# Kernel tuning notes

Hardware: AMD Instinct MI355X
Metric: run time of the kernel (lower is better)

Reference implementation:

```python
import jax, jax.numpy as jnp
import numpy as np

N = 96        # num_nodes
D = 64        # emb_size / n_hid
BS = 16
T = 13
G = 1         # num_graph

# all N^2 ordered pairs, receiver-major: edge e=i*N+j has receiver i, sender j
_REC = jnp.repeat(jnp.arange(N), N)
_SEND = jnp.tile(jnp.arange(N), N)


def _lin(shape, key, scale=0.05):
    return (jax.random.normal(key, shape, dtype=jnp.float32) * scale)


def setup_inputs() -> dict:
    key = jax.random.key(0)
    ks = jax.random.split(key, 24)
    inp = {
        "skill_seq": jax.random.randint(ks[0], (BS, T), 0, N, dtype=jnp.int32),
        "adj": jax.random.uniform(ks[1], (G, BS, N, N), dtype=jnp.float32),
        "node_embeddings": jax.random.normal(ks[2], (G, N, D), dtype=jnp.float32),
        # edge MLP
        "W_msg1": _lin((2 * D, D), ks[3]), "b_msg1": jnp.zeros((D,), jnp.float32),
        "W_msg2": _lin((D, D), ks[4]),     "b_msg2": jnp.zeros((D,), jnp.float32),
        # GRU hidden projections (no bias)
        "W_hr": _lin((D, D), ks[5]), "W_hi": _lin((D, D), ks[6]), "W_hh": _lin((D, D), ks[7]),
        # GRU input projections (bias)
        "W_ir": _lin((D, D), ks[8]),  "b_ir": jnp.zeros((D,), jnp.float32),
        "W_ii": _lin((D, D), ks[9]),  "b_ii": jnp.zeros((D,), jnp.float32),
        "W_in": _lin((D, D), ks[10]), "b_in": jnp.zeros((D,), jnp.float32),
        # output MLP
        "W_o1": _lin((D, D), ks[11]), "b_o1": jnp.zeros((D,), jnp.float32),
        "W_o2": _lin((D, D), ks[12]), "b_o2": jnp.zeros((D,), jnp.float32),
        "W_o3": _lin((D, D), ks[13]), "b_o3": jnp.zeros((D,), jnp.float32),
    }
    return inp


def _forward(skill_seq, adj, node_embeddings,
             W_msg1, b_msg1, W_msg2, b_msg2,
             W_hr, W_hi, W_hh,
             W_ir, b_ir, W_ii, b_ii, W_in, b_in,
             W_o1, b_o1, W_o2, b_o2, W_o3, b_o3):
    bs, time_steps = skill_seq.shape
    hidden0 = jnp.zeros((G, bs, N, D), dtype=adj.dtype)
    emb = node_embeddings[0]  # [N, D] (num_graph=1)

    def step(hidden, skill_t):
        # gather senders/receivers over the node axis -> [G, bs, N^2, 2D]
        senders = hidden[:, :, _SEND, :]
        receivers = hidden[:, :, _REC, :]
        pre_msg = jnp.concatenate([senders, receivers], axis=-1)
        msg = jnp.tanh(pre_msg @ W_msg1 + b_msg1)        # [G, bs, N^2, D]
        msg = jnp.tanh(msg @ W_msg2 + b_msg2)
        msg = msg.reshape(G, bs, N, N, D)                # receiver i, sender j
        # mask by adjacency and scatter-sum over senders, then /N
        agg = jnp.einsum('gbij,gbijd->gbid', adj, msg) / N   # [G, bs, N, D]
        inputs = emb[skill_t][None, :, None, :]          # [1, bs, 1, D]
        r = jax.nn.sigmoid(inputs @ W_ir + b_ir + agg @ W_hr)
        i = jax.nn.sigmoid(inputs @ W_ii + b_ii + agg @ W_hi)
        n = jnp.tanh(inputs @ W_in + b_in + r * (agg @ W_hh))
        hidden = (1.0 - i) * n + i * hidden
        pred = jax.nn.relu(hidden @ W_o1 + b_o1)
        pred = jax.nn.relu(pred @ W_o2 + b_o2)
        pred = pred @ W_o3 + b_o3                        # [G, bs, N, D]
        return hidden, pred

    skills_t = skill_seq[:, :time_steps - 1].T           # [T-1, bs]
    _, preds = jax.lax.scan(step, hidden0, skills_t)     # [T-1, G, bs, N, D]
    # torch: stack(dim=1) -> [G, T-1, bs, N, D]; transpose(1,2) -> [G, bs, T-1, N, D]
    return jnp.transpose(preds, (1, 2, 0, 3, 4))


def reference(skill_seq, adj, node_embeddings,
              W_msg1, b_msg1, W_msg2, b_msg2,
              W_hr, W_hi, W_hh,
              W_ir, b_ir, W_ii, b_ii, W_in, b_in,
              W_o1, b_o1, W_o2, b_o2, W_o3, b_o3):
    return _forward(skill_seq, adj, node_embeddings,
                    W_msg1, b_msg1, W_msg2, b_msg2,
                    W_hr, W_hi, W_hh,
                    W_ir, b_ir, W_ii, b_ii, W_in, b_in,
                    W_o1, b_o1, W_o2, b_o2, W_o3, b_o3)
```

## Files before the change

kernel.cpp:

```cpp
#include <hip/hip_runtime.h>

typedef unsigned short ushort_t;
typedef __attribute__((ext_vector_type(8))) short short8;
typedef __attribute__((ext_vector_type(8))) __bf16 bf16x8;
typedef __attribute__((ext_vector_type(4))) float floatx4;

#define NN 96
#define DD 64
#define BSZ 16
#define TSTEP 12
#define JSPLIT 8
#define JPW 12
#define ITILES 6

#define OFF_HALL  0u
#define OFF_E     5111808u
#define OFF_S0    5185536u
#define OFF_S1    5578752u
#define OFF_R0    5971968u
#define OFF_R1    6365184u
#define OFF_PART  6758400u
#define OFF_WSWZ  9904128u
#define OFF_CNT   9977856u
#define HSLOT     98304

union fragU  { short8 s; bf16x8 b; };
union packU  { floatx4 f; unsigned long long u[2]; };

static __device__ __forceinline__ short f2bf(float f){
    union { float f; unsigned u; } v; v.f = f;
    unsigned u = v.u;
    u += 0x7fffu + ((u >> 16) & 1u);
    return (short)(u >> 16);
}
static __device__ __forceinline__ float fast_tanh(float x){
    float p = __expf(2.f * x);
    return (p - 1.f) * __builtin_amdgcn_rcpf(p + 1.f);
}
static __device__ __forceinline__ float fast_sigmoid(float x){
    float p = __expf(-x);
    return __builtin_amdgcn_rcpf(1.f + p);
}
static __device__ __forceinline__ void zero4(floatx4* a){
    floatx4 z = {0.f,0.f,0.f,0.f};
    a[0]=z; a[1]=z; a[2]=z; a[3]=z;
}
static __device__ __forceinline__ void buildA(const float* sM, int col, int quad, short8& a0, short8& a1){
    floatx4 f0 = *(const floatx4*)&sM[col*68 + quad*8];
    floatx4 f1 = *(const floatx4*)&sM[col*68 + quad*8 + 4];
    floatx4 f2 = *(const floatx4*)&sM[col*68 + 32 + quad*8];
    floatx4 f3 = *(const floatx4*)&sM[col*68 + 32 + quad*8 + 4];
    fragU u0, u1;
    #pragma unroll
    for (int jj = 0; jj < 4; jj++){
        u0.b[jj]   = (__bf16)f0[jj];
        u0.b[4+jj] = (__bf16)f1[jj];
        u1.b[jj]   = (__bf16)f2[jj];
        u1.b[4+jj] = (__bf16)f3[jj];
    }
    a0 = u0.s; a1 = u1.s;
}
static __device__ __forceinline__ void mm16(short8 a0, short8 a1, const short8* wzm, int l, floatx4* acc){
    #pragma unroll
    for (int nt = 0; nt < 4; nt++){
        short8 b0 = wzm[nt*64 + l];
        short8 b1 = wzm[(4 + nt)*64 + l];
        acc[nt] = __builtin_amdgcn_mfma_f32_16x16x32_bf16(a0, b0, acc[nt], 0, 0, 0);
        acc[nt] = __builtin_amdgcn_mfma_f32_16x16x32_bf16(a1, b1, acc[nt], 0, 0, 0);
    }
}
static __device__ __forceinline__ void mm16r(short8 a0, short8 a1, const short8* f, floatx4* acc){
    #pragma unroll
    for (int nt = 0; nt < 4; nt++){
        acc[nt] = __builtin_amdgcn_mfma_f32_16x16x32_bf16(a0, f[nt],     acc[nt], 0, 0, 0);
        acc[nt] = __builtin_amdgcn_mfma_f32_16x16x32_bf16(a1, f[4 + nt], acc[nt], 0, 0, 0);
    }
}

__global__ __launch_bounds__(256) void k_init(
    const float* __restrict__ emb, const float* __restrict__ Wmsg1,
    const float* __restrict__ Wmsg2,
    const float* __restrict__ Whr, const float* __restrict__ Whi, const float* __restrict__ Whh,
    const float* __restrict__ Wir, const float* __restrict__ bir,
    const float* __restrict__ Wii, const float* __restrict__ bii,
    const float* __restrict__ Win, const float* __restrict__ bin,
    const float* __restrict__ Wo1, const float* __restrict__ Wo2, const float* __restrict__ Wo3,
    float* __restrict__ hz, float* __restrict__ S0, float* __restrict__ R0,
    int* __restrict__ cnt,
    float* __restrict__ Ef, ushort_t* __restrict__ wswz)
{
    int wg = blockIdx.x, tid = threadIdx.x;
    if (wg < 288) {
        int flat = wg*256 + tid;
        floatx4 z = {0.f,0.f,0.f,0.f};
        if      (flat < 24576) ((floatx4*)hz)[flat] = z;
        else if (flat < 49152) ((floatx4*)S0)[flat - 24576] = z;
        else                   ((floatx4*)R0)[flat - 49152] = z;
        if (wg < 5) {
            int c = wg*256 + tid;
            if (c < TSTEP*BSZ*ITILES) cnt[c] = 0;
        }
    } else if (wg < 360) {
        int flat = (wg - 288)*256 + tid;
        int m = flat / 6144; int r = flat % 6144; int s = r >> 6; int d = r & 63;
        const float* W = (m==0)? Wir : (m==1)? Wii : Win;
        const float* B = (m==0)? bir : (m==1)? bii : bin;
        float acc = B[d];
        #pragma unroll 8
        for (int k = 0; k < 64; k++)
            acc += emb[s*64 + k] * W[k*64 + d];
        Ef[flat] = acc;
    } else {
        int flat = (wg - 360)*256 + tid;
        int m = flat >> 12; int q = flat & 4095;
        int jj = q & 7, lane = (q >> 3) & 63, nt = (q >> 9) & 3, kc = q >> 11;
        int k = kc*32 + ((lane >> 4) << 3) + jj;
        int n = nt*16 + (lane & 15);
        const float* src; int idx = k*64 + n;
        switch (m) {
          case 0: src = Wmsg2; break;
          case 1: src = Whr;  break;
          case 2: src = Whi;  break;
          case 3: src = Whh;  break;
          case 4: src = Wmsg1; break;
          case 5: src = Wmsg1; idx = (64 + k)*64 + n; break;
          case 6: src = Wo1; break;
          case 7: src = Wo2; break;
          default: src = Wo3; break;
        }
        wswz[flat] = (ushort_t)f2bf(src[idx]);
    }
}

__global__ __launch_bounds__(256) void k_step(
    const float* __restrict__ adj, const float* __restrict__ b1in, const float* __restrict__ b2in,
    const float* __restrict__ Sread, const float* __restrict__ Rread,
    const ushort_t* __restrict__ wswz, float* __restrict__ partial,
    const int* __restrict__ skills, const float* __restrict__ Ef,
    const float* __restrict__ hprev, float* __restrict__ hcur,
    float* __restrict__ Swrite, float* __restrict__ Rwrite,
    int* __restrict__ cnt, int t)
{
    __shared__ float lds[6400];
    __shared__ int sLast;
    float* sS   = lds;
    float* sRB  = lds + 768;
    float* sAdj = lds + 1856;
    float* sAgg = lds + 2048;

    int wg = blockIdx.x;
    int js = wg / 96; int rem = wg % 96; int b = rem / 6; int it = rem % 6;
    int tid = threadIdx.x; int w = tid >> 6; int l = tid & 63;
    int quad = l >> 4, col = l & 15;
    int j0 = js * JPW;

    for (int q = tid; q < JPW*16; q += 256) {
        int row = q >> 4, c4 = (q & 15) * 4;
        *(floatx4*)&sS[row*64 + c4] = *(const floatx4*)&Sread[(b*NN + j0 + row)*64 + c4];
    }
    for (int q = tid; q < 16*16; q += 256) {
        int row = q >> 4, c4 = (q & 15) * 4;
        floatx4 r4 = *(const floatx4*)&Rread[(b*NN + it*16 + row)*64 + c4];
        floatx4 b4 = *(const floatx4*)&b1in[c4];
        floatx4 o = r4 + b4;
        *(floatx4*)&sRB[row*68 + c4] = o;
    }
    for (int q = tid; q < 16*JPW; q += 256) {
        int i = q / JPW, j = q % JPW;
        sAdj[q] = adj[(b*NN + it*16 + i)*NN + j0 + j];
    }
    const short8* wz = (const short8*)wswz;
    short8 w2f[2][4];
    #pragma unroll
    for (int kc = 0; kc < 2; kc++)
      #pragma unroll
      for (int nt = 0; nt < 4; nt++)
        w2f[kc][nt] = wz[(kc*4 + nt)*64 + l];
    float b2v[4];
    #pragma unroll
    for (int nt = 0; nt < 4; nt++) b2v[nt] = b2in[nt*16 + col];
    __syncthreads();

    float rbv[16];
    #pragma unroll
    for (int c = 0; c < 4; c++)
        *(floatx4*)&rbv[c*4] = *(const floatx4*)&sRB[col*68 + (c>>1)*32 + quad*8 + (c&1)*4];

    float agg[4][4];
    #pragma unroll
    for (int nt=0;nt<4;nt++)
      #pragma unroll
      for (int r=0;r<4;r++) agg[nt][r] = 0.f;

    for (int c = 0; c < 3; c++) {
        int jl = w*3 + c;
        float sv[16];
        #pragma unroll
        for (int cc = 0; cc < 4; cc++)
            *(floatx4*)&sv[cc*4] = *(const floatx4*)&sS[jl*64 + (cc>>1)*32 + quad*8 + (cc&1)*4];
        fragU u0, u1;
        #pragma unroll
        for (int e = 0; e < 8; e++) {
            u0.b[e] = (__bf16)fast_tanh(sv[e]   + rbv[e]);
            u1.b[e] = (__bf16)fast_tanh(sv[8+e] + rbv[8+e]);
        }
        floatx4 acc[4];
        zero4(acc);
        #pragma unroll
        for (int nt = 0; nt < 4; nt++) {
            acc[nt] = __builtin_amdgcn_mfma_f32_16x16x32_bf16(u0.s, w2f[0][nt], acc[nt], 0,0,0);
            acc[nt] = __builtin_amdgcn_mfma_f32_16x16x32_bf16(u1.s, w2f[1][nt], acc[nt], 0,0,0);
        }
        float adjv[4];
        #pragma unroll
        for (int r = 0; r < 4; r++) adjv[r] = sAdj[(quad*4 + r)*JPW + jl];
        #pragma unroll
        for (int nt = 0; nt < 4; nt++)
          #pragma unroll
          for (int r = 0; r < 4; r++)
            agg[nt][r] += adjv[r] * fast_tanh(acc[nt][r] + b2v[nt]);
    }
    #pragma unroll
    for (int nt = 0; nt < 4; nt++)
      #pragma unroll
      for (int r = 0; r < 4; r++)
        sAgg[w*1088 + (quad*4 + r)*68 + nt*16 + col] = agg[nt][r];
    __syncthreads();
    {
        int i = tid >> 4, k4 = (tid & 15) * 4;
        floatx4 s0 = *(const floatx4*)&sAgg[0*1088 + i*68 + k4];
        floatx4 s1 = *(const floatx4*)&sAgg[1*1088 + i*68 + k4];
        floatx4 s2 = *(const floatx4*)&sAgg[2*1088 + i*68 + k4];
        floatx4 s3 = *(const floatx4*)&sAgg[3*1088 + i*68 + k4];
        floatx4 o = (s0 + s1) + (s2 + s3);
        o = o * (1.f/96.f);
        packU pk; pk.f = o;
        unsigned long long* dst =
            (unsigned long long*)&partial[((js*BSZ + b)*NN + it*16 + i)*64 + k4];
        __hip_atomic_store(dst,     pk.u[0], __ATOMIC_RELAXED, __HIP_MEMORY_SCOPE_AGENT);
        __hip_atomic_store(dst + 1, pk.u[1], __ATOMIC_RELAXED, __HIP_MEMORY_SCOPE_AGENT);
    }
    if (t == TSTEP - 1) return;

    __syncthreads();
    if (tid == 0) {
        int old = atomicAdd(&cnt[t*(BSZ*ITILES) + b*ITILES + it], 1);
        sLast = (old == JSPLIT - 1);
    }
    __syncthreads();
    if (!sLast) return;

    float* sM = lds;
    float* sG = lds + 1088;
    float* sH = lds + 4352;
    float* sE = lds + 5376;

    const short8* wzb = (const short8*)wswz;
    short8 fG[8], fSR[8];
    if (w < 3) {
        #pragma unroll
        for (int q = 0; q < 8; q++) fG[q] = wzb[(1 + w)*512 + q*64 + l];
    }
    if (w < 2) {
        #pragma unroll
        for (int q = 0; q < 8; q++) fSR[q] = wzb[(4 + w)*512 + q*64 + l];
    }

    {
        int i = tid >> 4, k4 = (tid & 15) * 4;
        floatx4 a = {0.f,0.f,0.f,0.f};
        #pragma unroll
        for (int p = 0; p < JSPLIT; p++) {
            const unsigned long long* src =
                (const unsigned long long*)&partial[((p*BSZ + b)*NN + it*16 + i)*64 + k4];
            packU pk;
            pk.u[0] = __hip_atomic_load(src,     __ATOMIC_RELAXED, __HIP_MEMORY_SCOPE_AGENT);
            pk.u[1] = __hip_atomic_load(src + 1, __ATOMIC_RELAXED, __HIP_MEMORY_SCOPE_AGENT);
            a += pk.f;
        }
        *(floatx4*)&sM[i*68 + k4] = a;
        *(floatx4*)&sH[i*64 + k4] = *(const floatx4*)&hprev[(b*NN + it*16 + i)*64 + k4];
    }
    if (tid < 192) {
        int s = skills[b*13 + t];
        sE[tid] = Ef[(tid >> 6)*6144 + s*64 + (tid & 63)];
    }
    __syncthreads();

    if (w < 3) {
        short8 a0, a1;
        buildA(sM, col, quad, a0, a1);
        floatx4 acc[4];
        zero4(acc);
        mm16r(a0, a1, fG, acc);
        #pragma unroll
        for (int nt = 0; nt < 4; nt++)
          #pragma unroll
          for (int r = 0; r < 4; r++)
            sG[w*1088 + (quad*4 + r)*68 + nt*16 + col] = acc[nt][r];
    }
    __syncthreads();

    {
        int i = tid >> 4, k4 = (tid & 15) * 4;
        float h[4];
        #pragma unroll
        for (int e = 0; e < 4; e++) {
            int d = k4 + e;
            float gr = fast_sigmoid(sE[d]       + sG[0*1088 + i*68 + d]);
            float gi = fast_sigmoid(sE[64 + d]  + sG[1*1088 + i*68 + d]);
            float nv = fast_tanh  (sE[128 + d] + gr * sG[2*1088 + i*68 + d]);
            h[e] = (1.f - gi)*nv + gi*sH[i*64 + d];
        }
        #pragma unroll
        for (int e = 0; e < 4; e++) sM[i*68 + k4 + e] = h[e];
        floatx4 hv = { h[0], h[1], h[2], h[3] };
        *(floatx4*)&hcur[(b*NN + it*16 + i)*64 + k4] = hv;
    }
    __syncthreads();

    if (w < 2) {
        short8 a0, a1;
        buildA(sM, col, quad, a0, a1);
        floatx4 acc[4];
        zero4(acc);
        mm16r(a0, a1, fSR, acc);
        float* dst = (w == 0) ? Swrite : Rwrite;
        #pragma unroll
        for (int nt = 0; nt < 4; nt++)
          #pragma unroll
          for (int r = 0; r < 4; r++)
            dst[(b*NN + it*16 + quad*4 + r)*64 + nt*16 + col] = acc[nt][r];
    }
}

__global__ __launch_bounds__(256) void k_out(
    const int* __restrict__ skills, const float* __restrict__ partial,
    const float* __restrict__ Ef, const float* __restrict__ hall,
    const ushort_t* __restrict__ wswz,
    const float* __restrict__ bo1, const float* __restrict__ bo2, const float* __restrict__ bo3,
    float* __restrict__ out)
{
    __shared__ float sT[4][16*68];
    int tid = threadIdx.x; int w = tid >> 6; int l = tid & 63;
    int quad = l >> 4, col = l & 15;
    int g = blockIdx.x*4 + w;
    int ts = g / 96; int rem = g % 96; int b = rem / 6, it = rem % 6;
    float* sm = sT[w];

    if (ts < 11) {
        const float* hsrc = hall + (size_t)(ts + 1)*HSLOT + (b*NN + it*16)*64;
        int i = l >> 2, c0 = (l & 3)*16;
        #pragma unroll
        for (int cc = 0; cc < 4; cc++)
            *(floatx4*)&sm[i*68 + c0 + cc*4] = *(const floatx4*)&hsrc[i*64 + c0 + cc*4];
    } else {
        int i = l >> 2, c0 = (l & 3)*16;
        floatx4 a[4]; zero4(a);
        for (int p = 0; p < JSPLIT; p++) {
            const float* base = &partial[((p*BSZ + b)*NN + it*16 + i)*64 + c0];
            #pragma unroll
            for (int cc = 0; cc < 4; cc++) a[cc] += *(const floatx4*)&base[cc*4];
        }
        #pragma unroll
        for (int cc = 0; cc < 4; cc++) *(floatx4*)&sm[i*68 + c0 + cc*4] = a[cc];

        short8 a0, a1; buildA(sm, col, quad, a0, a1);
        floatx4 Ar[4], Ai[4], Ah[4];
        zero4(Ar); zero4(Ai); zero4(Ah);
        mm16(a0, a1, (const short8*)wswz + 1*512, l, Ar);
        mm16(a0, a1, (const short8*)wswz + 2*512, l, Ai);
        mm16(a0, a1, (const short8*)wswz + 3*512, l, Ah);
        int s = skills[b*13 + 11];
        const float* hp = hall + 11*(size_t)HSLOT;
        #pragma unroll
        for (int nt = 0; nt < 4; nt++) {
            int d = nt*16 + col;
            float er = Ef[0*6144 + s*64 + d];
            float ei = Ef[1*6144 + s*64 + d];
            float en = Ef[2*6144 + s*64 + d];
            #pragma unroll
            for (int r = 0; r < 4; r++) {
                int row = it*16 + quad*4 + r;
                float gr = fast_sigmoid(er + Ar[nt][r]);
                float gi = fast_sigmoid(ei + Ai[nt][r]);
                float nv = fast_tanh  (en + gr*Ah[nt][r]);
                sm[(quad*4 + r)*68 + d] = (1.f - gi)*nv + gi*hp[(b*NN + row)*64 + d];
            }
        }
    }

    float bv1[4], bv2[4], bv3[4];
    #pragma unroll
    for (int nt = 0; nt < 4; nt++) {
        bv1[nt] = bo1[nt*16 + col];
        bv2[nt] = bo2[nt*16 + col];
        bv3[nt] = bo3[nt*16 + col];
    }
    short8 a0, a1;
    floatx4 acc[4];

    buildA(sm, col, quad, a0, a1);
    zero4(acc);
    mm16(a0, a1, (const short8*)wswz + 6*512, l, acc);
    #pragma unroll
    for (int nt = 0; nt < 4; nt++)
      #pragma unroll
      for (int r = 0; r < 4; r++)
        sm[(quad*4 + r)*68 + nt*16 + col] = fmaxf(0.f, acc[nt][r] + bv1[nt]);

    buildA(sm, col, quad, a0, a1);
    zero4(acc);
    mm16(a0, a1, (const short8*)wswz + 7*512, l, acc);
    #pragma unroll
    for (int nt = 0; nt < 4; nt++)
      #pragma unroll
      for (int r = 0; r < 4; r++)
        sm[(quad*4 + r)*68 + nt*16 + col] = fmaxf(0.f, acc[nt][r] + bv2[nt]);

    buildA(sm, col, quad, a0, a1);
    zero4(acc);
    mm16(a0, a1, (const short8*)wswz + 8*512, l, acc);
    #pragma unroll
    for (int nt = 0; nt < 4; nt++)
      #pragma unroll
      for (int r = 0; r < 4; r++)
        out[((b*TSTEP + ts)*NN + it*16 + quad*4 + r)*64 + nt*16 + col] = acc[nt][r] + bv3[nt];
}

extern "C" void kernel_launch(void* const* d_in, const int* in_sizes, int n_in,
                              void* d_out, int out_size, void* d_ws, size_t ws_size,
                              hipStream_t stream) {
    const int*   skills = (const int*)d_in[0];
    const float* adj    = (const float*)d_in[1];
    const float* emb    = (const float*)d_in[2];
    const float* Wmsg1  = (const float*)d_in[3];
    const float* b1     = (const float*)d_in[4];
    const float* Wmsg2  = (const float*)d_in[5];
    const float* b2     = (const float*)d_in[6];
    const float* Whr    = (const float*)d_in[7];
    const float* Whi    = (const float*)d_in[8];
    const float* Whh    = (const float*)d_in[9];
    const float* Wir    = (const float*)d_in[10];
    const float* bir    = (const float*)d_in[11];
    const float* Wii    = (const float*)d_in[12];
    const float* bii    = (const float*)d_in[13];
    const float* Win    = (const float*)d_in[14];
    const float* bin    = (const float*)d_in[15];
    const float* Wo1    = (const float*)d_in[16];
    const float* bo1    = (const float*)d_in[17];
    const float* Wo2    = (const float*)d_in[18];
    const float* bo2    = (const float*)d_in[19];
    const float* Wo3    = (const float*)d_in[20];
    const float* bo3    = (const float*)d_in[21];

    char* ws = (char*)d_ws;
    float*    hall    = (float*)(ws + OFF_HALL);
    float*    Ef      = (float*)(ws + OFF_E);
    float*    S0      = (float*)(ws + OFF_S0);
    float*    S1      = (float*)(ws + OFF_S1);
    float*    R0      = (float*)(ws + OFF_R0);
    float*    R1      = (float*)(ws + OFF_R1);
    float*    partial = (float*)(ws + OFF_PART);
    ushort_t* wswz    = (ushort_t*)(ws + OFF_WSWZ);
    int*      cnt     = (int*)(ws + OFF_CNT);
    float*    out     = (float*)d_out;

    k_init<<<dim3(504), dim3(256), 0, stream>>>(emb, Wmsg1, Wmsg2, Whr, Whi, Whh,
        Wir, bir, Wii, bii, Win, bin, Wo1, Wo2, Wo3, hall, S0, R0, cnt, Ef, wswz);

    for (int t = 0; t < TSTEP; t++) {
        const float* Sr = (t & 1) ? S1 : S0;
        const float* Rr = (t & 1) ? R1 : R0;
        float*       Sw = (t & 1) ? S0 : S1;
        float*       Rw = (t & 1) ? R0 : R1;
        k_step<<<dim3(JSPLIT*BSZ*ITILES), dim3(256), 0, stream>>>(
            adj, b1, b2, Sr, Rr, wswz, partial, skills, Ef,
            hall + (size_t)t*HSLOT, hall + (size_t)(t+1)*HSLOT,
            Sw, Rw, cnt, t);
    }
    k_out<<<dim3(288), dim3(256), 0, stream>>>(skills, partial, Ef, hall, wswz,
        bo1, bo2, bo3, out);
}
```

Before: 255.5 us.

## Fuse per-timestep launches into one persistent kernel with tile-level flag synchronization

Replaces the twelve per-timestep k_step launches with a single persistent k_all kernel that loops over timesteps. Blocks wait on per-tile ready flags, published by the block that finishes the GRU update, instead of on kernel boundaries. S/R projections and hidden states are now kept per timestep rather than ping-ponged, and the initial zero state is synthesized in LDS. This removes launch gaps and full-grid barriers and lets independent tiles run ahead. The cost is spin-waiting, relaxed-atomic global traffic, and a reliance on all 768 blocks being co-resident (launch_bounds 256,3) to avoid deadlock.

```diff
diff --git a/kernel.cpp b/kernel.cpp
--- a/kernel.cpp
+++ b/kernel.cpp
@@ -12,16 +12,16 @@
 #define JSPLIT 8
 #define JPW 12
 #define ITILES 6
+#define NTILE (BSZ*ITILES)
 
 #define OFF_HALL  0u
 #define OFF_E     5111808u
-#define OFF_S0    5185536u
-#define OFF_S1    5578752u
-#define OFF_R0    5971968u
-#define OFF_R1    6365184u
-#define OFF_PART  6758400u
-#define OFF_WSWZ  9904128u
-#define OFF_CNT   9977856u
+#define OFF_SG    5185536u
+#define OFF_RG    9904128u
+#define OFF_PART  14622720u
+#define OFF_WSWZ  17768448u
+#define OFF_CNT   17842176u
+#define OFF_FLAG  17846784u
 #define HSLOT     98304
 
 union fragU  { short8 s; bf16x8 b; };
@@ -44,6 +44,19 @@
 static __device__ __forceinline__ void zero4(floatx4* a){
     floatx4 z = {0.f,0.f,0.f,0.f};
     a[0]=z; a[1]=z; a[2]=z; a[3]=z;
+}
+static __device__ __forceinline__ floatx4 aload4(const float* p){
+    const unsigned long long* s = (const unsigned long long*)p;
+    packU pk;
+    pk.u[0] = __hip_atomic_load(s,     __ATOMIC_RELAXED, __HIP_MEMORY_SCOPE_AGENT);
+    pk.u[1] = __hip_atomic_load(s + 1, __ATOMIC_RELAXED, __HIP_MEMORY_SCOPE_AGENT);
+    return pk.f;
+}
+static __device__ __forceinline__ void astore4(float* p, floatx4 v){
+    unsigned long long* d = (unsigned long long*)p;
+    packU pk; pk.f = v;
+    __hip_atomic_store(d,     pk.u[0], __ATOMIC_RELAXED, __HIP_MEMORY_SCOPE_AGENT);
+    __hip_atomic_store(d + 1, pk.u[1], __ATOMIC_RELAXED, __HIP_MEMORY_SCOPE_AGENT);
 }
 static __device__ __forceinline__ void buildA(const float* sM, int col, int quad, short8& a0, short8& a1){
     floatx4 f0 = *(const floatx4*)&sM[col*68 + quad*8];
@@ -85,23 +98,19 @@
     const float* __restrict__ Wii, const float* __restrict__ bii,
     const float* __restrict__ Win, const float* __restrict__ bin,
     const float* __restrict__ Wo1, const float* __restrict__ Wo2, const float* __restrict__ Wo3,
-    float* __restrict__ hz, float* __restrict__ S0, float* __restrict__ R0,
-    int* __restrict__ cnt,
+    float* __restrict__ hz, int* __restrict__ cntflag,
     float* __restrict__ Ef, ushort_t* __restrict__ wswz)
 {
     int wg = blockIdx.x, tid = threadIdx.x;
-    if (wg < 288) {
-        int flat = wg*256 + tid;
+    if (wg < 96) {
         floatx4 z = {0.f,0.f,0.f,0.f};
-        if      (flat < 24576) ((floatx4*)hz)[flat] = z;
-        else if (flat < 49152) ((floatx4*)S0)[flat - 24576] = z;
-        else                   ((floatx4*)R0)[flat - 49152] = z;
-        if (wg < 5) {
+        ((floatx4*)hz)[wg*256 + tid] = z;
+        if (wg < 9) {
             int c = wg*256 + tid;
-            if (c < TSTEP*BSZ*ITILES) cnt[c] = 0;
-        }
-    } else if (wg < 360) {
-        int flat = (wg - 288)*256 + tid;
+            if (c < 2304) cntflag[c] = 0;
+        }
+    } else if (wg < 168) {
+        int flat = (wg - 96)*256 + tid;
         int m = flat / 6144; int r = flat % 6144; int s = r >> 6; int d = r & 63;
         const float* W = (m==0)? Wir : (m==1)? Wii : Win;
         const float* B = (m==0)? bir : (m==1)? bii : bin;
@@ -111,7 +120,7 @@
             acc += emb[s*64 + k] * W[k*64 + d];
         Ef[flat] = acc;
     } else {
-        int flat = (wg - 360)*256 + tid;
+        int flat = (wg - 168)*256 + tid;
         int m = flat >> 12; int q = flat & 4095;
         int jj = q & 7, lane = (q >> 3) & 63, nt = (q >> 9) & 3, kc = q >> 11;
         int k = kc*32 + ((lane >> 4) << 3) + jj;
@@ -132,39 +141,31 @@
     }
 }
 
-__global__ __launch_bounds__(256) void k_step(
+__global__ __launch_bounds__(256, 3) void k_all(
     const float* __restrict__ adj, const float* __restrict__ b1in, const float* __restrict__ b2in,
-    const float* __restrict__ Sread, const float* __restrict__ Rread,
-    const ushort_t* __restrict__ wswz, float* __restrict__ partial,
     const int* __restrict__ skills, const float* __restrict__ Ef,
-    const float* __restrict__ hprev, float* __restrict__ hcur,
-    float* __restrict__ Swrite, float* __restrict__ Rwrite,
-    int* __restrict__ cnt, int t)
+    const ushort_t* __restrict__ wswz,
+    float* __restrict__ partial, float* __restrict__ Sbuf, float* __restrict__ Rbuf,
+    float* __restrict__ hall, int* __restrict__ cnt, int* __restrict__ flagv)
 {
-    __shared__ float lds[6400];
+    __shared__ float lds[7616];
     __shared__ int sLast;
     float* sS   = lds;
     float* sRB  = lds + 768;
     float* sAdj = lds + 1856;
     float* sAgg = lds + 2048;
+    float* sM = lds + 2048;
+    float* sG = lds + 3136;
+    float* sH = lds + 6400;
+    float* sE = lds + 7424;
 
     int wg = blockIdx.x;
     int js = wg / 96; int rem = wg % 96; int b = rem / 6; int it = rem % 6;
     int tid = threadIdx.x; int w = tid >> 6; int l = tid & 63;
     int quad = l >> 4, col = l & 15;
     int j0 = js * JPW;
-
-    for (int q = tid; q < JPW*16; q += 256) {
-        int row = q >> 4, c4 = (q & 15) * 4;
-        *(floatx4*)&sS[row*64 + c4] = *(const floatx4*)&Sread[(b*NN + j0 + row)*64 + c4];
-    }
-    for (int q = tid; q < 16*16; q += 256) {
-        int row = q >> 4, c4 = (q & 15) * 4;
-        floatx4 r4 = *(const floatx4*)&Rread[(b*NN + it*16 + row)*64 + c4];
-        floatx4 b4 = *(const floatx4*)&b1in[c4];
-        floatx4 o = r4 + b4;
-        *(floatx4*)&sRB[row*68 + c4] = o;
-    }
+    int jt0 = j0 >> 4, jt1 = (j0 + JPW - 1) >> 4;
+
     for (int q = tid; q < 16*JPW; q += 256) {
         int i = q / JPW, j = q % JPW;
         sAdj[q] = adj[(b*NN + it*16 + i)*NN + j0 + j];
@@ -179,158 +180,176 @@
     float b2v[4];
     #pragma unroll
     for (int nt = 0; nt < 4; nt++) b2v[nt] = b2in[nt*16 + col];
-    __syncthreads();
-
-    float rbv[16];
-    #pragma unroll
-    for (int c = 0; c < 4; c++)
-        *(floatx4*)&rbv[c*4] = *(const floatx4*)&sRB[col*68 + (c>>1)*32 + quad*8 + (c&1)*4];
-
-    float agg[4][4];
-    #pragma unroll
-    for (int nt=0;nt<4;nt++)
-      #pragma unroll
-      for (int r=0;r<4;r++) agg[nt][r] = 0.f;
-
-    for (int c = 0; c < 3; c++) {
-        int jl = w*3 + c;
-        float sv[16];
-        #pragma unroll
-        for (int cc = 0; cc < 4; cc++)
-            *(floatx4*)&sv[cc*4] = *(const floatx4*)&sS[jl*64 + (cc>>1)*32 + quad*8 + (cc&1)*4];
-        fragU u0, u1;
-        #pragma unroll
-        for (int e = 0; e < 8; e++) {
-            u0.b[e] = (__bf16)fast_tanh(sv[e]   + rbv[e]);
-            u1.b[e] = (__bf16)fast_tanh(sv[8+e] + rbv[8+e]);
-        }
-        floatx4 acc[4];
-        zero4(acc);
-        #pragma unroll
-        for (int nt = 0; nt < 4; nt++) {
-            acc[nt] = __builtin_amdgcn_mfma_f32_16x16x32_bf16(u0.s, w2f[0][nt], acc[nt], 0,0,0);
-            acc[nt] = __builtin_amdgcn_mfma_f32_16x16x32_bf16(u1.s, w2f[1][nt], acc[nt], 0,0,0);
-        }
-        float adjv[4];
-        #pragma unroll
-        for (int r = 0; r < 4; r++) adjv[r] = sAdj[(quad*4 + r)*JPW + jl];
+
+    for (int t = 0; t < TSTEP; t++) {
+        if (t == 0) {
+            for (int q = tid; q < JPW*64; q += 256) sS[q] = 0.f;
+            for (int q = tid; q < 16*64; q += 256) sRB[(q >> 6)*68 + (q & 63)] = b1in[q & 63];
+        } else {
+            if (tid < 3) {
+                int tile = (tid == 0) ? it : (tid == 1) ? jt0 : jt1;
+                const int* fp = &flagv[t*NTILE + b*ITILES + tile];
+                while (__hip_atomic_load(fp, __ATOMIC_RELAXED, __HIP_MEMORY_SCOPE_AGENT) == 0)
+                    __builtin_amdgcn_s_sleep(2);
+            }
+            __syncthreads();
+            const float* St = Sbuf + (size_t)t*HSLOT;
+            const float* Rt = Rbuf + (size_t)t*HSLOT;
+            for (int q = tid; q < JPW*16; q += 256) {
+                int row = q >> 4, c4 = (q & 15)*4;
+                *(floatx4*)&sS[row*64 + c4] = aload4(&St[(b*NN + j0 + row)*64 + c4]);
+            }
+            for (int q = tid; q < 16*16; q += 256) {
+                int row = q >> 4, c4 = (q & 15)*4;
+                floatx4 r4 = aload4(&Rt[(b*NN + it*16 + row)*64 + c4]);
+                floatx4 b4 = *(const floatx4*)&b1in[c4];
+                *(floatx4*)&sRB[row*68 + c4] = r4 + b4;
+            }
+        }
+        __syncthreads();
+
+        float rbv[16];
+        #pragma unroll
+        for (int c = 0; c < 4; c++)
+            *(floatx4*)&rbv[c*4] = *(const floatx4*)&sRB[col*68 + (c>>1)*32 + quad*8 + (c&1)*4];
+
+        float agg[4][4];
+        #pragma unroll
+        for (int nt=0;nt<4;nt++)
+          #pragma unroll
+          for (int r=0;r<4;r++) agg[nt][r] = 0.f;
+
+        for (int c = 0; c < 3; c++) {
+            int jl = w*3 + c;
+            float sv[16];
+            #pragma unroll
+            for (int cc = 0; cc < 4; cc++)
+                *(floatx4*)&sv[cc*4] = *(const floatx4*)&sS[jl*64 + (cc>>1)*32 + quad*8 + (cc&1)*4];
+            fragU u0, u1;
+            #pragma unroll
+            for (int e = 0; e < 8; e++) {
+                u0.b[e] = (__bf16)fast_tanh(sv[e]   + rbv[e]);
+                u1.b[e] = (__bf16)fast_tanh(sv[8+e] + rbv[8+e]);
+            }
+            floatx4 acc[4];
+            zero4(acc);
+            #pragma unroll
+            for (int nt = 0; nt < 4; nt++) {
+                acc[nt] = __builtin_amdgcn_mfma_f32_16x16x32_bf16(u0.s, w2f[0][nt], acc[nt], 0,0,0);
+                acc[nt] = __builtin_amdgcn_mfma_f32_16x16x32_bf16(u1.s, w2f[1][nt], acc[nt], 0,0,0);
+            }
+            float adjv[4];
+            #pragma unroll
+            for (int r = 0; r < 4; r++) adjv[r] = sAdj[(quad*4 + r)*JPW + jl];
+            #pragma unroll
+            for (int nt = 0; nt < 4; nt++)
+              #pragma unroll
+              for (int r = 0; r < 4; r++)
+                agg[nt][r] += adjv[r] * fast_tanh(acc[nt][r] + b2v[nt]);
+        }
         #pragma unroll
         for (int nt = 0; nt < 4; nt++)
           #pragma unroll
           for (int r = 0; r < 4; r++)
-            agg[nt][r] += adjv[r] * fast_tanh(acc[nt][r] + b2v[nt]);
-    }
-    #pragma unroll
-    for (int nt = 0; nt < 4; nt++)
-      #pragma unroll
-      for (int r = 0; r < 4; r++)
-        sAgg[w*1088 + (quad*4 + r)*68 + nt*16 + col] = agg[nt][r];
-    __syncthreads();
-    {
-        int i = tid >> 4, k4 = (tid & 15) * 4;
-        floatx4 s0 = *(const floatx4*)&sAgg[0*1088 + i*68 + k4];
-        floatx4 s1 = *(const floatx4*)&sAgg[1*1088 + i*68 + k4];
-        floatx4 s2 = *(const floatx4*)&sAgg[2*1088 + i*68 + k4];
-        floatx4 s3 = *(const floatx4*)&sAgg[3*1088 + i*68 + k4];
-        floatx4 o = (s0 + s1) + (s2 + s3);
-        o = o * (1.f/96.f);
-        packU pk; pk.f = o;
-        unsigned long long* dst =
-            (unsigned long long*)&partial[((js*BSZ + b)*NN + it*16 + i)*64 + k4];
-        __hip_atomic_store(dst,     pk.u[0], __ATOMIC_RELAXED, __HIP_MEMORY_SCOPE_AGENT);
-        __hip_atomic_store(dst + 1, pk.u[1], __ATOMIC_RELAXED, __HIP_MEMORY_SCOPE_AGENT);
-    }
-    if (t == TSTEP - 1) return;
-
-    __syncthreads();
-    if (tid == 0) {
-        int old = atomicAdd(&cnt[t*(BSZ*ITILES) + b*ITILES + it], 1);
-        sLast = (old == JSPLIT - 1);
-    }
-    __syncthreads();
-    if (!sLast) return;
-
-    float* sM = lds;
-    float* sG = lds + 1088;
-    float* sH = lds + 4352;
-    float* sE = lds + 5376;
-
-    const short8* wzb = (const short8*)wswz;
-    short8 fG[8], fSR[8];
-    if (w < 3) {
-        #pragma unroll
-        for (int q = 0; q < 8; q++) fG[q] = wzb[(1 + w)*512 + q*64 + l];
-    }
-    if (w < 2) {
-        #pragma unroll
-        for (int q = 0; q < 8; q++) fSR[q] = wzb[(4 + w)*512 + q*64 + l];
-    }
-
-    {
-        int i = tid >> 4, k4 = (tid & 15) * 4;
-        floatx4 a = {0.f,0.f,0.f,0.f};
-        #pragma unroll
-        for (int p = 0; p < JSPLIT; p++) {
-            const unsigned long long* src =
-                (const unsigned long long*)&partial[((p*BSZ + b)*NN + it*16 + i)*64 + k4];
-            packU pk;
-            pk.u[0] = __hip_atomic_load(src,     __ATOMIC_RELAXED, __HIP_MEMORY_SCOPE_AGENT);
-            pk.u[1] = __hip_atomic_load(src + 1, __ATOMIC_RELAXED, __HIP_MEMORY_SCOPE_AGENT);
-            a += pk.f;
-        }
-        *(floatx4*)&sM[i*68 + k4] = a;
-        *(floatx4*)&sH[i*64 + k4] = *(const floatx4*)&hprev[(b*NN + it*16 + i)*64 + k4];
-    }
-    if (tid < 192) {
-        int s = skills[b*13 + t];
-        sE[tid] = Ef[(tid >> 6)*6144 + s*64 + (tid & 63)];
-    }
-    __syncthreads();
-
-    if (w < 3) {
-        short8 a0, a1;
-        buildA(sM, col, quad, a0, a1);
-        floatx4 acc[4];
-        zero4(acc);
-        mm16r(a0, a1, fG, acc);
-        #pragma unroll
-        for (int nt = 0; nt < 4; nt++)
-          #pragma unroll
-          for (int r = 0; r < 4; r++)
-            sG[w*1088 + (quad*4 + r)*68 + nt*16 + col] = acc[nt][r];
-    }
-    __syncthreads();
-
-    {
-        int i = tid >> 4, k4 = (tid & 15) * 4;
-        float h[4];
-        #pragma unroll
-        for (int e = 0; e < 4; e++) {
-            int d = k4 + e;
-            float gr = fast_sigmoid(sE[d]       + sG[0*1088 + i*68 + d]);
-            float gi = fast_sigmoid(sE[64 + d]  + sG[1*1088 + i*68 + d]);
-            float nv = fast_tanh  (sE[128 + d] + gr * sG[2*1088 + i*68 + d]);
-            h[e] = (1.f - gi)*nv + gi*sH[i*64 + d];
-        }
-        #pragma unroll
-        for (int e = 0; e < 4; e++) sM[i*68 + k4 + e] = h[e];
-        floatx4 hv = { h[0], h[1], h[2], h[3] };
-        *(floatx4*)&hcur[(b*NN + it*16 + i)*64 + k4] = hv;
-    }
-    __syncthreads();
-
-    if (w < 2) {
-        short8 a0, a1;
-        buildA(sM, col, quad, a0, a1);
-        floatx4 acc[4];
-        zero4(acc);
-        mm16r(a0, a1, fSR, acc);
-        float* dst = (w == 0) ? Swrite : Rwrite;
-        #pragma unroll
-        for (int nt = 0; nt < 4; nt++)
-          #pragma unroll
-          for (int r = 0; r < 4; r++)
-            dst[(b*NN + it*16 + quad*4 + r)*64 + nt*16 + col] = acc[nt][r];
+            sAgg[w*1088 + (quad*4 + r)*68 + nt*16 + col] = agg[nt][r];
+        __syncthreads();
+        {
+            int i = tid >> 4, k4 = (tid & 15)*4;
+            floatx4 s0 = *(const floatx4*)&sAgg[0*1088 + i*68 + k4];
+            floatx4 s1 = *(const floatx4*)&sAgg[1*1088 + i*68 + k4];
+            floatx4 s2 = *(const floatx4*)&sAgg[2*1088 + i*68 + k4];
+            floatx4 s3 = *(const floatx4*)&sAgg[3*1088 + i*68 + k4];
+            floatx4 o = (s0 + s1) + (s2 + s3);
+            o = o * (1.f/96.f);
+            astore4(&partial[((js*BSZ + b)*NN + it*16 + i)*64 + k4], o);
+        }
+        if (t == TSTEP - 1) break;
+
+        __syncthreads();
+        if (tid == 0) {
+            int old = atomicAdd(&cnt[t*NTILE + b*ITILES + it], 1);
+            sLast = (old == JSPLIT - 1);
+        }
+        __syncthreads();
+
+        if (sLast) {
+            const short8* wzb = (const short8*)wswz;
+            short8 fG[8], fSR[8];
+            if (w < 3) {
+                #pragma unroll
+                for (int q = 0; q < 8; q++) fG[q] = wzb[(1 + w)*512 + q*64 + l];
+            }
+            if (w < 2) {
+                #pragma unroll
+                for (int q = 0; q < 8; q++) fSR[q] = wzb[(4 + w)*512 + q*64 + l];
+            }
+            {
+                int i = tid >> 4, k4 = (tid & 15)*4;
+                floatx4 a = {0.f,0.f,0.f,0.f};
+                #pragma unroll
+                for (int p = 0; p < JSPLIT; p++)
+                    a += aload4(&partial[((p*BSZ + b)*NN + it*16 + i)*64 + k4]);
+                *(floatx4*)&sM[i*68 + k4] = a;
+                *(floatx4*)&sH[i*64 + k4] =
+                    aload4(&hall[(size_t)t*HSLOT + (b*NN + it*16 + i)*64 + k4]);
+            }
+            if (tid < 192) {
+                int s = skills[b*13 + t];
+                sE[tid] = Ef[(tid >> 6)*6144 + s*64 + (tid & 63)];
+            }
+            __syncthreads();
+
+            if (w < 3) {
+                short8 a0, a1;
+                buildA(sM, col, quad, a0, a1);
+                floatx4 acc[4];
+                zero4(acc);
+                mm16r(a0, a1, fG, acc);
+                #pragma unroll
+                for (int nt = 0; nt < 4; nt++)
+                  #pragma unroll
+                  for (int r = 0; r < 4; r++)
+                    sG[w*1088 + (quad*4 + r)*68 + nt*16 + col] = acc[nt][r];
+            }
+            __syncthreads();
+
+            {
+                int i = tid >> 4, k4 = (tid & 15)*4;
+                float h[4];
+                #pragma unroll
+                for (int e = 0; e < 4; e++) {
+                    int d = k4 + e;
+                    float gr = fast_sigmoid(sE[d]       + sG[0*1088 + i*68 + d]);
+                    float gi = fast_sigmoid(sE[64 + d]  + sG[1*1088 + i*68 + d]);
+                    float nv = fast_tanh  (sE[128 + d] + gr * sG[2*1088 + i*68 + d]);
+                    h[e] = (1.f - gi)*nv + gi*sH[i*64 + d];
+                }
+                #pragma unroll
+                for (int e = 0; e < 4; e++) sM[i*68 + k4 + e] = h[e];
+                floatx4 hv = { h[0], h[1], h[2], h[3] };
+                astore4(&hall[(size_t)(t+1)*HSLOT + (b*NN + it*16 + i)*64 + k4], hv);
+            }
+            __syncthreads();
+
+            if (w < 2) {
+                short8 a0, a1;
+                buildA(sM, col, quad, a0, a1);
+                floatx4 acc[4];
+                zero4(acc);
+                mm16r(a0, a1, fSR, acc);
+                float* dst = ((w == 0) ? Sbuf : Rbuf) + (size_t)(t+1)*HSLOT;
+                #pragma unroll
+                for (int nt = 0; nt < 4; nt++)
+                  #pragma unroll
+                  for (int r = 0; r < 4; r++)
+                    __hip_atomic_store(&dst[(b*NN + it*16 + quad*4 + r)*64 + nt*16 + col],
+                                       acc[nt][r], __ATOMIC_RELAXED, __HIP_MEMORY_SCOPE_AGENT);
+            }
+            __syncthreads();
+            if (tid == 0)
+                __hip_atomic_store(&flagv[(t+1)*NTILE + b*ITILES + it], 1,
+                                   __ATOMIC_RELAXED, __HIP_MEMORY_SCOPE_AGENT);
+        }
     }
 }
 
@@ -457,28 +476,20 @@
     char* ws = (char*)d_ws;
     float*    hall    = (float*)(ws + OFF_HALL);
     float*    Ef      = (float*)(ws + OFF_E);
-    float*    S0      = (float*)(ws + OFF_S0);
-    float*    S1      = (float*)(ws + OFF_S1);
-    float*    R0      = (float*)(ws + OFF_R0);
-    float*    R1      = (float*)(ws + OFF_R1);
+    float*    Sbuf    = (float*)(ws + OFF_SG);
+    float*    Rbuf    = (float*)(ws + OFF_RG);
     float*    partial = (float*)(ws + OFF_PART);
     ushort_t* wswz    = (ushort_t*)(ws + OFF_WSWZ);
     int*      cnt     = (int*)(ws + OFF_CNT);
+    int*      flagv   = (int*)(ws + OFF_FLAG);
     float*    out     = (float*)d_out;
 
-    k_init<<<dim3(504), dim3(256), 0, stream>>>(emb, Wmsg1, Wmsg2, Whr, Whi, Whh,
-        Wir, bir, Wii, bii, Win, bin, Wo1, Wo2, Wo3, hall, S0, R0, cnt, Ef, wswz);
-
-    for (int t = 0; t < TSTEP; t++) {
-        const float* Sr = (t & 1) ? S1 : S0;
-        const float* Rr = (t & 1) ? R1 : R0;
-        float*       Sw = (t & 1) ? S0 : S1;
-        float*       Rw = (t & 1) ? R0 : R1;
-        k_step<<<dim3(JSPLIT*BSZ*ITILES), dim3(256), 0, stream>>>(
-            adj, b1, b2, Sr, Rr, wswz, partial, skills, Ef,
-            hall + (size_t)t*HSLOT, hall + (size_t)(t+1)*HSLOT,
-            Sw, Rw, cnt, t);
-    }
+    k_init<<<dim3(312), dim3(256), 0, stream>>>(emb, Wmsg1, Wmsg2, Whr, Whi, Whh,
+        Wir, bir, Wii, bii, Win, bin, Wo1, Wo2, Wo3, hall, cnt, Ef, wswz);
+
+    k_all<<<dim3(JSPLIT*BSZ*ITILES), dim3(256), 0, stream>>>(
+        adj, b1, b2, skills, Ef, wswz, partial, Sbuf, Rbuf, hall, cnt, flagv);
+
     k_out<<<dim3(288), dim3(256), 0, stream>>>(skills, partial, Ef, hall, wswz,
         bo1, bo2, bo3, out);
 }
```

After: 421.4 us. 65.0% more time.

## Specialize first recurrence step using zero initial hidden state

Applied to the files above, without the earlier changes.

Adds a dedicated k_step0 kernel that exploits the zero initial hidden state. Every edge message at step 0 is then the same vector, tanh(W2·tanh(b1)+b2), so aggregation reduces to adjacency row sums times that vector. This replaces a full 768-block edge-MLP pass with a 96-block kernel, and drops the zero-fill of hidden, S0 and R0 from k_init. It also fully unrolls the per-wave chunk loop in k_step and moves the atomic partial loads and stores into helpers. The risk is that any later read of the no-longer-zeroed hall slot 0 would see stale data.

```diff
diff --git a/kernel.cpp b/kernel.cpp
--- a/kernel.cpp
+++ b/kernel.cpp
@@ -45,6 +45,19 @@
     floatx4 z = {0.f,0.f,0.f,0.f};
     a[0]=z; a[1]=z; a[2]=z; a[3]=z;
 }
+static __device__ __forceinline__ floatx4 aload4(const float* p){
+    const unsigned long long* s = (const unsigned long long*)p;
+    packU pk;
+    pk.u[0] = __hip_atomic_load(s,     __ATOMIC_RELAXED, __HIP_MEMORY_SCOPE_AGENT);
+    pk.u[1] = __hip_atomic_load(s + 1, __ATOMIC_RELAXED, __HIP_MEMORY_SCOPE_AGENT);
+    return pk.f;
+}
+static __device__ __forceinline__ void astore4(float* p, floatx4 v){
+    unsigned long long* d = (unsigned long long*)p;
+    packU pk; pk.f = v;
+    __hip_atomic_store(d,     pk.u[0], __ATOMIC_RELAXED, __HIP_MEMORY_SCOPE_AGENT);
+    __hip_atomic_store(d + 1, pk.u[1], __ATOMIC_RELAXED, __HIP_MEMORY_SCOPE_AGENT);
+}
 static __device__ __forceinline__ void buildA(const float* sM, int col, int quad, short8& a0, short8& a1){
     floatx4 f0 = *(const floatx4*)&sM[col*68 + quad*8];
     floatx4 f1 = *(const floatx4*)&sM[col*68 + quad*8 + 4];
@@ -85,23 +98,11 @@
     const float* __restrict__ Wii, const float* __restrict__ bii,
     const float* __restrict__ Win, const float* __restrict__ bin,
     const float* __restrict__ Wo1, const float* __restrict__ Wo2, const float* __restrict__ Wo3,
-    float* __restrict__ hz, float* __restrict__ S0, float* __restrict__ R0,
-    int* __restrict__ cnt,
-    float* __restrict__ Ef, ushort_t* __restrict__ wswz)
+    int* __restrict__ cnt, float* __restrict__ Ef, ushort_t* __restrict__ wswz)
 {
     int wg = blockIdx.x, tid = threadIdx.x;
-    if (wg < 288) {
+    if (wg < 72) {
         int flat = wg*256 + tid;
-        floatx4 z = {0.f,0.f,0.f,0.f};
-        if      (flat < 24576) ((floatx4*)hz)[flat] = z;
-        else if (flat < 49152) ((floatx4*)S0)[flat - 24576] = z;
-        else                   ((floatx4*)R0)[flat - 49152] = z;
-        if (wg < 5) {
-            int c = wg*256 + tid;
-            if (c < TSTEP*BSZ*ITILES) cnt[c] = 0;
-        }
-    } else if (wg < 360) {
-        int flat = (wg - 288)*256 + tid;
         int m = flat / 6144; int r = flat % 6144; int s = r >> 6; int d = r & 63;
         const float* W = (m==0)? Wir : (m==1)? Wii : Win;
         const float* B = (m==0)? bir : (m==1)? bii : bin;
@@ -110,8 +111,12 @@
         for (int k = 0; k < 64; k++)
             acc += emb[s*64 + k] * W[k*64 + d];
         Ef[flat] = acc;
+        if (wg < 5) {
+            int c = wg*256 + tid;
+            if (c < TSTEP*BSZ*ITILES) cnt[c] = 0;
+        }
     } else {
-        int flat = (wg - 360)*256 + tid;
+        int flat = (wg - 72)*256 + tid;
         int m = flat >> 12; int q = flat & 4095;
         int jj = q & 7, lane = (q >> 3) & 63, nt = (q >> 9) & 3, kc = q >> 11;
         int k = kc*32 + ((lane >> 4) << 3) + jj;
@@ -132,6 +137,111 @@
     }
 }
 
+__global__ __launch_bounds__(256) void k_step0(
+    const float* __restrict__ adj, const float* __restrict__ b1in, const float* __restrict__ b2in,
+    const int* __restrict__ skills, const float* __restrict__ Ef,
+    const ushort_t* __restrict__ wswz,
+    float* __restrict__ hall, float* __restrict__ S1, float* __restrict__ R1)
+{
+    __shared__ float sM[16*68];
+    __shared__ float sG[3][16*68];
+    __shared__ float sE[3*64];
+    __shared__ float sRS[16*17];
+    int wg = blockIdx.x; int b = wg / 6, it = wg % 6;
+    int tid = threadIdx.x; int w = tid >> 6; int l = tid & 63;
+    int quad = l >> 4, col = l & 15;
+
+    {
+        int i = tid >> 4, seg = tid & 15;
+        const float* arow = &adj[(b*NN + it*16 + i)*NN + seg*6];
+        float s = 0.f;
+        #pragma unroll
+        for (int j = 0; j < 6; j++) s += arow[j];
+        sRS[i*17 + seg] = s;
+    }
+    if (tid < 192) {
+        int s = skills[b*13 + 0];
+        sE[tid] = Ef[(tid >> 6)*6144 + s*64 + (tid & 63)];
+    }
+    __syncthreads();
+    if (tid < 16) {
+        float s = 0.f;
+        #pragma unroll
+        for (int q = 0; q < 16; q++) s += sRS[tid*17 + q];
+        sRS[tid*17 + 16] = s * (1.f/96.f);
+    }
+    __syncthreads();
+
+    if (w == 0) {
+        float b2v[4];
+        #pragma unroll
+        for (int nt = 0; nt < 4; nt++) b2v[nt] = b2in[nt*16 + col];
+        fragU u0, u1;
+        #pragma unroll
+        for (int e = 0; e < 8; e++) {
+            u0.b[e] = (__bf16)fast_tanh(b1in[quad*8 + e]);
+            u1.b[e] = (__bf16)fast_tanh(b1in[32 + quad*8 + e]);
+        }
+        floatx4 acc[4];
+        zero4(acc);
+        mm16(u0.s, u1.s, (const short8*)wswz + 0*512, l, acc);
+        #pragma unroll
+        for (int nt = 0; nt < 4; nt++)
+          #pragma unroll
+          for (int r = 0; r < 4; r++) {
+            float m = fast_tanh(acc[nt][r] + b2v[nt]);
+            sM[(quad*4 + r)*68 + nt*16 + col] = sRS[(quad*4 + r)*17 + 16] * m;
+          }
+    }
+    __syncthreads();
+
+    if (w < 3) {
+        short8 a0, a1;
+        buildA(sM, col, quad, a0, a1);
+        floatx4 acc[4];
+        zero4(acc);
+        mm16(a0, a1, (const short8*)wswz + (1 + w)*512, l, acc);
+        #pragma unroll
+        for (int nt = 0; nt < 4; nt++)
+          #pragma unroll
+          for (int r = 0; r < 4; r++)
+            sG[w][(quad*4 + r)*68 + nt*16 + col] = acc[nt][r];
+    }
+    __syncthreads();
+
+    {
+        int i = tid >> 4, k4 = (tid & 15)*4;
+        float h[4];
+        #pragma unroll
+        for (int e = 0; e < 4; e++) {
+            int d = k4 + e;
+            float gi = fast_sigmoid(sE[64 + d] + sG[1][i*68 + d]);
+            float gr = fast_sigmoid(sE[d]      + sG[0][i*68 + d]);
+            float nv = fast_tanh  (sE[128 + d] + gr * sG[2][i*68 + d]);
+            h[e] = (1.f - gi)*nv;
+        }
+        #pragma unroll
+        for (int e = 0; e < 4; e++) sM[i*68 + k4 + e] = h[e];
+        floatx4 hv = { h[0], h[1], h[2], h[3] };
+        *(floatx4*)&hall[(size_t)1*HSLOT + (b*NN + it*16 + i)*64 + k4] = hv;
+    }
+    __syncthreads();
+
+    if (w < 2) {
+        short8 a0, a1;
+        buildA(sM, col, quad, a0, a1);
+        floatx4 acc[4];
+        zero4(acc);
+        mm16(a0, a1, (const short8*)wswz + (4 + w)*512, l, acc);
+        float* dst = (w == 0) ? S1 : R1;
+        #pragma unroll
+        for (int nt = 0; nt < 4; nt++)
+          #pragma unroll
+          for (int r = 0; r < 4; r++)
+            dst[(b*NN + it*16 + quad*4 + r)*64 + nt*16 + col] = acc[nt][r];
+    }
+}
+
 __global__ __launch_bounds__(256) void k_step(
     const float* __restrict__ adj, const float* __restrict__ b1in, const float* __restrict__ b2in,
     const float* __restrict__ Sread, const float* __restrict__ Rread,
@@ -192,6 +302,7 @@
       #pragma unroll
       for (int r=0;r<4;r++) agg[nt][r] = 0.f;
 
+    #pragma unroll
     for (int c = 0; c < 3; c++) {
         int jl = w*3 + c;
         float sv[16];
@@ -234,11 +345,7 @@
         floatx4 s3 = *(const floatx4*)&sAgg[3*1088 + i*68 + k4];
         floatx4 o = (s0 + s1) + (s2 + s3);
         o = o * (1.f/96.f);
-        packU pk; pk.f = o;
-        unsigned long long* dst =
-            (unsigned long long*)&partial[((js*BSZ + b)*NN + it*16 + i)*64 + k4];
-        __hip_atomic_store(dst,     pk.u[0], __ATOMIC_RELAXED, __HIP_MEMORY_SCOPE_AGENT);
-        __hip_atomic_store(dst + 1, pk.u[1], __ATOMIC_RELAXED, __HIP_MEMORY_SCOPE_AGENT);
+        astore4(&partial[((js*BSZ + b)*NN + it*16 + i)*64 + k4], o);
     }
     if (t == TSTEP - 1) return;
 
@@ -270,14 +377,8 @@
         int i = tid >> 4, k4 = (tid & 15) * 4;
         floatx4 a = {0.f,0.f,0.f,0.f};
         #pragma unroll
-        for (int p = 0; p < JSPLIT; p++) {
-            const unsigned long long* src =
-                (const unsigned long long*)&partial[((p*BSZ + b)*NN + it*16 + i)*64 + k4];
-            packU pk;
-            pk.u[0] = __hip_atomic_load(src,     __ATOMIC_RELAXED, __HIP_MEMORY_SCOPE_AGENT);
-            pk.u[1] = __hip_atomic_load(src + 1, __ATOMIC_RELAXED, __HIP_MEMORY_SCOPE_AGENT);
-            a += pk.f;
-        }
+        for (int p = 0; p < JSPLIT; p++)
+            a += aload4(&partial[((p*BSZ + b)*NN + it*16 + i)*64 + k4]);
         *(floatx4*)&sM[i*68 + k4] = a;
         *(floatx4*)&sH[i*64 + k4] = *(const floatx4*)&hprev[(b*NN + it*16 + i)*64 + k4];
     }
@@ -466,10 +567,13 @@
     int*      cnt     = (int*)(ws + OFF_CNT);
     float*    out     = (float*)d_out;
 
-    k_init<<<dim3(504), dim3(256), 0, stream>>>(emb, Wmsg1, Wmsg2, Whr, Whi, Whh,
-        Wir, bir, Wii, bii, Win, bin, Wo1, Wo2, Wo3, hall, S0, R0, cnt, Ef, wswz);
-
-    for (int t = 0; t < TSTEP; t++) {
+    k_init<<<dim3(216), dim3(256), 0, stream>>>(emb, Wmsg1, Wmsg2, Whr, Whi, Whh,
+        Wir, bir, Wii, bii, Win, bin, Wo1, Wo2, Wo3, cnt, Ef, wswz);
+
+    k_step0<<<dim3(BSZ*ITILES), dim3(256), 0, stream>>>(
+        adj, b1, b2, skills, Ef, wswz, hall, S1, R1);
+
+    for (int t = 1; t < TSTEP; t++) {
         const float* Sr = (t & 1) ? S1 : S0;
         const float* Rr = (t & 1) ? R1 : R0;
         float*       Sw = (t & 1) ? S0 : S1;
```

Result: no change. 252.4 us (-1.2%).
